# Kernel tuning notes

Measured on AMD Instinct MI355X. Metric: run time of the kernel, lower is better.

Reference implementation:

```python
import jax, jax.numpy as jnp
import numpy as np

N_NODES = 50000
N_EDGES = 800000  # undirected unique edges (i < j)
D = 64


def setup_inputs() -> dict:
    key = jax.random.key(0)
    ks = jax.random.split(key, 8)
    # Build a deduplicated undirected edge list with i < j so that the
    # symmetrized edge list exactly matches the dense 0/1 adjacency semantics
    # of the original module (duplicates would double-count in segment_sum).
    rng = np.random.default_rng(0)
    a = rng.integers(0, N_NODES, size=4 * N_EDGES, dtype=np.int64)
    b = rng.integers(0, N_NODES, size=4 * N_EDGES, dtype=np.int64)
    lo, hi = np.minimum(a, b), np.maximum(a, b)
    mask = lo != hi  # drop self loops (adj diagonal would be set, but keep it simple/undirected)
    pairs = np.unique(np.stack([lo[mask], hi[mask]], axis=1), axis=0)
    pairs = pairs[:N_EDGES]
    edge_index = jnp.asarray(pairs.T)  # [2, E]

    s = 0.05
    return {
        "h": jax.random.normal(ks[0], (N_NODES, D), dtype=jnp.float32),
        "edge_index": edge_index,
        "att_w": jax.random.normal(ks[1], (2 * D, 2), dtype=jnp.float32) * s,
        "att_b": jnp.zeros((2,), dtype=jnp.float32),
        "w1": jax.random.normal(ks[2], (D, D), dtype=jnp.float32) * s,
        "b1": jnp.zeros((D,), dtype=jnp.float32),
        "w2": jax.random.normal(ks[3], (D, D), dtype=jnp.float32) * s,
        "b2": jnp.zeros((D,), dtype=jnp.float32),
        "w3": jax.random.normal(ks[4], (D, D), dtype=jnp.float32) * s,
        "b3": jnp.zeros((D,), dtype=jnp.float32),
    }


def reference(h, edge_index, att_w, att_b, w1, b1, w2, b2, w3, b3):
    n = h.shape[0]
    # Symmetrize: adjacency is set in both directions in the original code.
    rows = jnp.concatenate([edge_index[0], edge_index[1]])  # destination nodes
    cols = jnp.concatenate([edge_index[1], edge_index[0]])  # neighbor sources

    gathered = h[cols]  # [2E, D]
    agg_sum = jax.ops.segment_sum(gathered, rows, num_segments=n)
    agg_max = jax.ops.segment_max(gathered, rows, num_segments=n)
    deg = jax.ops.segment_sum(jnp.ones_like(rows, dtype=h.dtype), rows, num_segments=n)
    # Nodes with no neighbors stay at zero in the original (loop is skipped).
    agg_max = jnp.where(deg[:, None] > 0, agg_max, jnp.zeros_like(agg_max))
    # (mean aggregation in the original is computed but never used -> omitted)

    # Attention over (sum, max) aggregations
    scores = jnp.concatenate([agg_sum, agg_max], axis=1) @ att_w + att_b  # [N, 2]
    weights = jax.nn.softmax(scores, axis=1)
    att_out = weights[:, 0:1] * agg_sum + weights[:, 1:2] * agg_max

    x = h + att_out
    # MLP(in_dim, hidden=out_dim, out_dim, hidden_layers=2)
    x = jax.nn.relu(x @ w1 + b1)
    x = jax.nn.relu(x @ w2 + b2)
    return x @ w3 + b3
```

## Files before the change

### kernel.cpp

```cpp
#include <hip/hip_runtime.h>
#include <math.h>
#include <float.h>

#define N_NODES 50000
#define N_EDGES 800000
#define D 64

#define NCH 1024
#define CHUNK 782
#define PART_SHIFT 9
#define PROWS 512
#define NPART_B 98
#define CNT_LEN (NPART_B * NCH)

static inline size_t align_up(size_t x, size_t a) { return (x + a - 1) & ~(a - 1); }

__global__ void k_offsA(const int* __restrict__ e0, int* __restrict__ offsA) {
    int v = blockIdx.x * blockDim.x + threadIdx.x;
    if (v > N_NODES) return;
    int lo = 0, hi = N_EDGES;
    while (lo < hi) {
        int mid = (lo + hi) >> 1;
        if (e0[mid] < v) lo = mid + 1; else hi = mid;
    }
    offsA[v] = lo;
}

__global__ __launch_bounds__(256) void k_count(const int* __restrict__ e1,
                                               int* __restrict__ countsG) {
    __shared__ int cnt[NPART_B];
    for (int i = threadIdx.x; i < NPART_B; i += 256) cnt[i] = 0;
    __syncthreads();
    int s = blockIdx.x * CHUNK;
    int e = min(s + CHUNK, N_EDGES);
    for (int j = s + threadIdx.x; j < e; j += 256)
        atomicAdd(&cnt[e1[j] >> PART_SHIFT], 1);
    __syncthreads();
    for (int p = threadIdx.x; p < NPART_B; p += 256)
        countsG[p * NCH + blockIdx.x] = cnt[p];
}

__global__ void k_scan1(const int* __restrict__ deg, int* __restrict__ offs,
                        int* __restrict__ bsum, int L) {
    __shared__ int s[1024];
    int tid = threadIdx.x;
    int i = blockIdx.x * 1024 + tid;
    int v = (i < L) ? deg[i] : 0;
    s[tid] = v;
    __syncthreads();
    for (int d = 1; d < 1024; d <<= 1) {
        int t = (tid >= d) ? s[tid - d] : 0;
        __syncthreads();
        v += t;
        s[tid] = v;
        __syncthreads();
    }
    if (i < L) offs[i + 1] = v;
    if (tid == 1023) bsum[blockIdx.x] = v;
}

__global__ void k_scan2(int* __restrict__ bsum, int nb) {
    __shared__ int s[128];
    int tid = threadIdx.x;
    if (tid < nb) s[tid] = bsum[tid];
    __syncthreads();
    if (tid == 0) {
        int run = 0;
        for (int b = 0; b < nb; ++b) { int t = s[b]; s[b] = run; run += t; }
    }
    __syncthreads();
    if (tid < nb) bsum[tid] = s[tid];
}

__global__ void k_scan3(int* __restrict__ offs, const int* __restrict__ bsum, int L) {
    int i = blockIdx.x * blockDim.x + threadIdx.x;
    if (i == 0) offs[0] = 0;
    if (i < L) offs[i + 1] += bsum[i >> 10];
}

__global__ __launch_bounds__(256) void k_scatter(const int* __restrict__ e0,
                                                 const int* __restrict__ e1,
                                                 const int* __restrict__ cbase,
                                                 unsigned* __restrict__ bucket) {
    __shared__ int cur[NPART_B];
    for (int i = threadIdx.x; i < NPART_B; i += 256)
        cur[i] = cbase[i * NCH + blockIdx.x];
    __syncthreads();
    int s = blockIdx.x * CHUNK;
    int e = min(s + CHUNK, N_EDGES);
    for (int j = s + threadIdx.x; j < e; j += 256) {
        int hi = e1[j], lo = e0[j];
        int pos = atomicAdd(&cur[hi >> PART_SHIFT], 1);
        bucket[pos] = ((unsigned)hi << 16) | (unsigned)lo;
    }
}

__global__ __launch_bounds__(1024) void k_csrB(const unsigned* __restrict__ bucket,
                                               const int* __restrict__ cbase,
                                               int* __restrict__ offsB,
                                               int* __restrict__ adjB) {
    __shared__ int bins[PROWS];
    __shared__ int excl[PROWS];
    __shared__ int cur[PROWS];
    int p = blockIdx.x;
    int segS = cbase[p * NCH];
    int segE = (p + 1 < NPART_B) ? cbase[(p + 1) * NCH] : N_EDGES;
    int r0 = p << PART_SHIFT;
    for (int i = threadIdx.x; i < PROWS; i += 1024) bins[i] = 0;
    __syncthreads();
    for (int j = segS + threadIdx.x; j < segE; j += 1024)
        atomicAdd(&bins[(int)(bucket[j] >> 16) - r0], 1);
    __syncthreads();
    if (threadIdx.x < PROWS) excl[threadIdx.x] = bins[threadIdx.x];
    __syncthreads();
    for (int d = 1; d < PROWS; d <<= 1) {
        int t = 0;
        if (threadIdx.x < PROWS && threadIdx.x >= d) t = excl[threadIdx.x - d];
        __syncthreads();
        if (threadIdx.x < PROWS) excl[threadIdx.x] += t;
        __syncthreads();
    }
    if (threadIdx.x < PROWS) {
        int st = segS + excl[threadIdx.x] - bins[threadIdx.x];
        cur[threadIdx.x] = st;
        int v = r0 + threadIdx.x;
        if (v < N_NODES) offsB[v] = st;
    }
    if (p == NPART_B - 1 && threadIdx.x == 0) offsB[N_NODES] = N_EDGES;
    __syncthreads();
    for (int j = segS + threadIdx.x; j < segE; j += 1024) {
        unsigned pk = bucket[j];
        int pos = atomicAdd(&cur[(int)(pk >> 16) - r0], 1);
        adjB[pos] = (int)(pk & 0xFFFFu);
    }
}

__global__ void k_agg(const float* __restrict__ h, const int* __restrict__ offsA,
                      const int* __restrict__ e1, const int* __restrict__ offsB,
                      const int* __restrict__ adjB, const float* __restrict__ att_w,
                      const float* __restrict__ att_b, float* __restrict__ xbuf) {
    int wid = (blockIdx.x * blockDim.x + threadIdx.x) >> 6;
    int lane = threadIdx.x & 63;
    int sA = offsA[wid], eA = offsA[wid + 1];
    int sB = offsB[wid], eB = offsB[wid + 1];
    float sum = 0.f, mx = -FLT_MAX;
    for (int pass = 0; pass < 2; ++pass) {
        const int* lst = pass ? adjB : e1;
        int e = pass ? sB : sA;
        int end = pass ? eB : eA;
        for (; e + 4 <= end; e += 4) {
            int c0 = lst[e], c1 = lst[e + 1], c2 = lst[e + 2], c3 = lst[e + 3];
            float v0 = h[c0 * D + lane];
            float v1 = h[c1 * D + lane];
            float v2 = h[c2 * D + lane];
            float v3 = h[c3 * D + lane];
            sum += v0 + v1 + v2 + v3;
            mx = fmaxf(mx, fmaxf(fmaxf(v0, v1), fmaxf(v2, v3)));
        }
        for (; e < end; ++e) {
            float v = h[lst[e] * D + lane];
            sum += v;
            mx = fmaxf(mx, v);
        }
    }
    if ((eA - sA) + (eB - sB) == 0) mx = 0.f;

    float aw00 = att_w[lane * 2 + 0], aw01 = att_w[lane * 2 + 1];
    float aw10 = att_w[(D + lane) * 2 + 0], aw11 = att_w[(D + lane) * 2 + 1];
    float p0 = sum * aw00 + mx * aw10;
    float p1 = sum * aw01 + mx * aw11;
    for (int o = 32; o > 0; o >>= 1) {
        p0 += __shfl_xor(p0, o);
        p1 += __shfl_xor(p1, o);
    }
    float s0 = p0 + att_b[0], s1 = p1 + att_b[1];
    float m = fmaxf(s0, s1);
    float e0v = expf(s0 - m), e1v = expf(s1 - m);
    float inv = 1.f / (e0v + e1v);
    float w0 = e0v * inv, w1 = e1v * inv;
    xbuf[wid * D + lane] = h[wid * D + lane] + w0 * sum + w1 * mx;
}

__global__ __launch_bounds__(256) void k_dense(const float* __restrict__ xbuf,
        const float* __restrict__ w1, const float* __restrict__ b1,
        const float* __restrict__ w2, const float* __restrict__ b2,
        const float* __restrict__ w3, const float* __restrict__ b3,
        float* __restrict__ out) {
    __shared__ float xt[64 * 64];
    __shared__ float yt[64 * 64];
    __shared__ float wb[64 * 64];
    int tid = threadIdx.x;
    int base = blockIdx.x * 64;

    for (int i = tid; i < 64 * 64; i += 256) {
        int r = base + (i >> 6);
        xt[i] = (r < N_NODES) ? xbuf[(size_t)base * 64 + i] : 0.f;
    }
    for (int i = tid; i < 64 * 64; i += 256) wb[i] = w1[i];
    __syncthreads();

    int wave = tid >> 6, lane = tid & 63;
    float bias = b1[lane];
    for (int rr = 0; rr < 16; ++rr) {
        int r = wave * 16 + rr;
        float acc = bias;
#pragma unroll
        for (int k = 0; k < 64; ++k) acc += xt[r * 64 + k] * wb[k * 64 + lane];
        yt[r * 64 + lane] = fmaxf(acc, 0.f);
    }
    __syncthreads();
    for (int i = tid; i < 64 * 64; i += 256) wb[i] = w2[i];
    __syncthreads();
    bias = b2[lane];
    for (int rr = 0; rr < 16; ++rr) {
        int r = wave * 16 + rr;
        float acc = bias;
#pragma unroll
        for (int k = 0; k < 64; ++k) acc += yt[r * 64 + k] * wb[k * 64 + lane];
        xt[r * 64 + lane] = fmaxf(acc, 0.f);
    }
    __syncthreads();
    for (int i = tid; i < 64 * 64; i += 256) wb[i] = w3[i];
    __syncthreads();
    bias = b3[lane];
    for (int rr = 0; rr < 16; ++rr) {
        int r = wave * 16 + rr;
        int gr = base + r;
        if (gr >= N_NODES) continue;
        float acc = bias;
#pragma unroll
        for (int k = 0; k < 64; ++k) acc += xt[r * 64 + k] * wb[k * 64 + lane];
        out[(size_t)gr * 64 + lane] = acc;
    }
}

extern "C" void kernel_launch(void* const* d_in, const int* in_sizes, int n_in,
                              void* d_out, int out_size, void* d_ws, size_t ws_size,
                              hipStream_t stream) {
    const float* h     = (const float*)d_in[0];
    const int*   ei    = (const int*)d_in[1];
    const float* att_w = (const float*)d_in[2];
    const float* att_b = (const float*)d_in[3];
    const float* w1    = (const float*)d_in[4];
    const float* b1    = (const float*)d_in[5];
    const float* w2    = (const float*)d_in[6];
    const float* b2    = (const float*)d_in[7];
    const float* w3    = (const float*)d_in[8];
    const float* b3    = (const float*)d_in[9];
    float* out = (float*)d_out;

    const int* e0 = ei;
    const int* e1 = ei + N_EDGES;

    char* ws = (char*)d_ws;
    size_t off = 0;
    auto alloc = [&](size_t bytes) {
        char* p = ws + off;
        off = align_up(off + bytes, 256);
        return p;
    };
    int* offsA       = (int*)alloc((size_t)(N_NODES + 1) * 4);
    int* countsG     = (int*)alloc((size_t)CNT_LEN * 4);
    int* cbase       = (int*)alloc((size_t)(CNT_LEN + 1) * 4);
    int* bsum        = (int*)alloc(128 * 4);
    unsigned* bucket = (unsigned*)alloc((size_t)N_EDGES * 4);
    int* offsB       = (int*)alloc((size_t)(N_NODES + 1) * 4);
    int* adjB        = (int*)alloc((size_t)N_EDGES * 4);
    float* xbuf      = out;

    int nbc = CNT_LEN / 1024;
    k_offsA  <<<(N_NODES + 256) / 256, 256, 0, stream>>>(e0, offsA);
    k_count  <<<NCH, 256, 0, stream>>>(e1, countsG);
    k_scan1  <<<nbc, 1024, 0, stream>>>(countsG, cbase, bsum, CNT_LEN);
    k_scan2  <<<1, 128, 0, stream>>>(bsum, nbc);
    k_scan3  <<<(CNT_LEN + 255) / 256, 256, 0, stream>>>(cbase, bsum, CNT_LEN);
    k_scatter<<<NCH, 256, 0, stream>>>(e0, e1, cbase, bucket);
    k_csrB   <<<NPART_B, 1024, 0, stream>>>(bucket, cbase, offsB, adjB);
    k_agg    <<<(N_NODES * 64) / 256, 256, 0, stream>>>(h, offsA, e1, offsB, adjB,
                                                        att_w, att_b, xbuf);
    k_dense  <<<(N_NODES + 63) / 64, 256, 0, stream>>>(xbuf, w1, b1, w2, b2, w3, b3, out);
}
```

Baseline: 235.4 us.

## Register-resident MLP weights with lane broadcasts; unroll gather loop by eight

```diff
diff --git a/kernel.cpp b/kernel.cpp
--- a/kernel.cpp
+++ b/kernel.cpp
@@ -14,6 +14,10 @@
 #define CNT_LEN (NPART_B * NCH)
 
 static inline size_t align_up(size_t x, size_t a) { return (x + a - 1) & ~(a - 1); }
+
+__device__ __forceinline__ float lane_bcast(float v, int k) {
+    return __uint_as_float(__builtin_amdgcn_readlane(__float_as_uint(v), k));
+}
 
 __global__ void k_offsA(const int* __restrict__ e0, int* __restrict__ offsA) {
     int v = blockIdx.x * blockDim.x + threadIdx.x;
@@ -148,14 +152,20 @@
         const int* lst = pass ? adjB : e1;
         int e = pass ? sB : sA;
         int end = pass ? eB : eA;
-        for (; e + 4 <= end; e += 4) {
-            int c0 = lst[e], c1 = lst[e + 1], c2 = lst[e + 2], c3 = lst[e + 3];
+        for (; e + 8 <= end; e += 8) {
+            int c0 = lst[e],     c1 = lst[e + 1], c2 = lst[e + 2], c3 = lst[e + 3];
+            int c4 = lst[e + 4], c5 = lst[e + 5], c6 = lst[e + 6], c7 = lst[e + 7];
             float v0 = h[c0 * D + lane];
             float v1 = h[c1 * D + lane];
             float v2 = h[c2 * D + lane];
             float v3 = h[c3 * D + lane];
-            sum += v0 + v1 + v2 + v3;
-            mx = fmaxf(mx, fmaxf(fmaxf(v0, v1), fmaxf(v2, v3)));
+            float v4 = h[c4 * D + lane];
+            float v5 = h[c5 * D + lane];
+            float v6 = h[c6 * D + lane];
+            float v7 = h[c7 * D + lane];
+            sum += ((v0 + v1) + (v2 + v3)) + ((v4 + v5) + (v6 + v7));
+            mx = fmaxf(mx, fmaxf(fmaxf(fmaxf(v0, v1), fmaxf(v2, v3)),
+                                 fmaxf(fmaxf(v4, v5), fmaxf(v6, v7))));
         }
         for (; e < end; ++e) {
             float v = h[lst[e] * D + lane];
@@ -186,51 +196,49 @@
         const float* __restrict__ w2, const float* __restrict__ b2,
         const float* __restrict__ w3, const float* __restrict__ b3,
         float* __restrict__ out) {
-    __shared__ float xt[64 * 64];
-    __shared__ float yt[64 * 64];
-    __shared__ float wb[64 * 64];
-    int tid = threadIdx.x;
-    int base = blockIdx.x * 64;
-
-    for (int i = tid; i < 64 * 64; i += 256) {
-        int r = base + (i >> 6);
-        xt[i] = (r < N_NODES) ? xbuf[(size_t)base * 64 + i] : 0.f;
-    }
-    for (int i = tid; i < 64 * 64; i += 256) wb[i] = w1[i];
-    __syncthreads();
-
-    int wave = tid >> 6, lane = tid & 63;
+    int gwave = (blockIdx.x * blockDim.x + threadIdx.x) >> 6;
+    int lane  = threadIdx.x & 63;
+    int r0 = gwave * 16;
+    if (r0 >= N_NODES) return;
+
+    float w[64];
+#pragma unroll
+    for (int k = 0; k < 64; ++k) w[k] = w1[(k << 6) + lane];
+
+    float x16[16];
+#pragma unroll
+    for (int r = 0; r < 16; ++r) x16[r] = xbuf[(size_t)(r0 + r) * 64 + lane];
+
+    float y[16];
     float bias = b1[lane];
-    for (int rr = 0; rr < 16; ++rr) {
-        int r = wave * 16 + rr;
-        float acc = bias;
-#pragma unroll
-        for (int k = 0; k < 64; ++k) acc += xt[r * 64 + k] * wb[k * 64 + lane];
-        yt[r * 64 + lane] = fmaxf(acc, 0.f);
-    }
-    __syncthreads();
-    for (int i = tid; i < 64 * 64; i += 256) wb[i] = w2[i];
-    __syncthreads();
+#pragma unroll
+    for (int r = 0; r < 16; ++r) {
+        float a = bias;
+#pragma unroll
+        for (int k = 0; k < 64; ++k) a += lane_bcast(x16[r], k) * w[k];
+        y[r] = fmaxf(a, 0.f);
+    }
+
+#pragma unroll
+    for (int k = 0; k < 64; ++k) w[k] = w2[(k << 6) + lane];
     bias = b2[lane];
-    for (int rr = 0; rr < 16; ++rr) {
-        int r = wave * 16 + rr;
-        float acc = bias;
-#pragma unroll
-        for (int k = 0; k < 64; ++k) acc += yt[r * 64 + k] * wb[k * 64 + lane];
-        xt[r * 64 + lane] = fmaxf(acc, 0.f);
-    }
-    __syncthreads();
-    for (int i = tid; i < 64 * 64; i += 256) wb[i] = w3[i];
-    __syncthreads();
+#pragma unroll
+    for (int r = 0; r < 16; ++r) {
+        float a = bias;
+#pragma unroll
+        for (int k = 0; k < 64; ++k) a += lane_bcast(y[r], k) * w[k];
+        x16[r] = fmaxf(a, 0.f);
+    }
+
+#pragma unroll
+    for (int k = 0; k < 64; ++k) w[k] = w3[(k << 6) + lane];
     bias = b3[lane];
-    for (int rr = 0; rr < 16; ++rr) {
-        int r = wave * 16 + rr;
-        int gr = base + r;
-        if (gr >= N_NODES) continue;
-        float acc = bias;
-#pragma unroll
-        for (int k = 0; k < 64; ++k) acc += xt[r * 64 + k] * wb[k * 64 + lane];
-        out[(size_t)gr * 64 + lane] = acc;
+#pragma unroll
+    for (int r = 0; r < 16; ++r) {
+        float a = bias;
+#pragma unroll
+        for (int k = 0; k < 64; ++k) a += lane_bcast(x16[r], k) * w[k];
+        out[(size_t)(r0 + r) * 64 + lane] = a;
     }
 }
 
@@ -278,5 +286,5 @@
     k_csrB   <<<NPART_B, 1024, 0, stream>>>(bucket, cbase, offsB, adjB);
     k_agg    <<<(N_NODES * 64) / 256, 256, 0, stream>>>(h, offsA, e1, offsB, adjB,
                                                         att_w, att_b, xbuf);
-    k_dense  <<<(N_NODES + 63) / 64, 256, 0, stream>>>(xbuf, w1, b1, w2, b2, w3, b3, out);
-}
+    k_dense  <<<(3125 + 3) / 4, 256, 0, stream>>>(xbuf, w1, b1, w2, b2, w3, b3, out);
+}
```

Result: faster. 215.4 us (-8.5%).
